# Optimization experiments

Hardware: AMD Instinct MI355X
Metric: run time of the kernel (lower is better)

## Reference

```python
import jax, jax.numpy as jnp
import numpy as np

B, N, HID, H = 16, 256, 512, 8
DK = HID // H          # att_size = 64
FEAT = 8               # storage/operator feature dim
MLP_H = 64             # interaction MLP hidden dim
LAM = 0.1              # htap_lambda
SCALE = DK ** -0.5


def _pair_bias(feat, W1, b1, W2, b2):
    """MLP([v_i || v_j || |v_i - v_j|]) for all pairs -> [B,N,N,H].
    Split W1 over the three concat blocks so the per-node parts are O(N)."""
    F = feat.shape[-1]
    Wa, Wb, Wc = W1[:F], W1[F:2 * F], W1[2 * F:]
    hi = feat @ Wa                                    # [B,N,MLP_H]
    hj = feat @ Wb                                    # [B,N,MLP_H]
    diff = jnp.abs(feat[:, :, None, :] - feat[:, None, :, :])  # [B,N,N,F]
    h = jax.nn.relu(hi[:, :, None, :] + hj[:, None, :, :] + diff @ Wc + b1)
    return h @ W2 + b2                                # [B,N,N,H]


def setup_inputs() -> dict:
    key = jax.random.key(0)
    ks = jax.random.split(key, 24)
    g = lambda i, shape, s=0.05: jax.random.normal(ks[i], shape, jnp.float32) * (1.0 if s is None else 1.0) * (s / 0.05 * 0.05 if False else 1.0)
    def w(i, shape, scale):
        return jax.random.normal(ks[i], shape, jnp.float32) * scale
    inp = {
        "q": w(0, (B, N, HID), 1.0),
        "k": w(1, (B, N, HID), 1.0),
        "v": w(2, (B, N, HID), 1.0),
        "tree_attn_bias": w(3, (B, H, N, N), 1.0),
        "storage_features": w(4, (B, N, FEAT), 1.0),
        "operator_features": w(5, (B, N, FEAT), 1.0),
        # attention projections (stored as [in,out])
        "Wq": w(6, (HID, HID), HID ** -0.5), "bq": jnp.zeros((HID,), jnp.float32),
        "Wk": w(7, (HID, HID), HID ** -0.5), "bk": jnp.zeros((HID,), jnp.float32),
        "Wv": w(8, (HID, HID), HID ** -0.5), "bv": jnp.zeros((HID,), jnp.float32),
        "Wo": w(9, (HID, HID), HID ** -0.5), "bo": jnp.zeros((HID,), jnp.float32),
        # f_s interaction MLP: Linear(3*FEAT,64) -> ReLU -> Linear(64,H)
        "fs_W1": w(10, (3 * FEAT, MLP_H), (3 * FEAT) ** -0.5), "fs_b1": jnp.zeros((MLP_H,), jnp.float32),
        "fs_W2": w(11, (MLP_H, H), MLP_H ** -0.5), "fs_b2": jnp.zeros((H,), jnp.float32),
        # f_o interaction MLP
        "fo_W1": w(12, (3 * FEAT, MLP_H), (3 * FEAT) ** -0.5), "fo_b1": jnp.zeros((MLP_H,), jnp.float32),
        "fo_W2": w(13, (MLP_H, H), MLP_H ** -0.5), "fo_b2": jnp.zeros((H,), jnp.float32),
    }
    return inp


def reference(q, k, v, tree_attn_bias, storage_features, operator_features,
              Wq, bq, Wk, bk, Wv, bv, Wo, bo,
              fs_W1, fs_b1, fs_W2, fs_b2, fo_W1, fo_b1, fo_W2, fo_b2):
    # projections -> [B,H,N,DK]
    qh = (q @ Wq + bq).reshape(B, N, H, DK).transpose(0, 2, 1, 3) * SCALE
    kh = (k @ Wk + bk).reshape(B, N, H, DK).transpose(0, 2, 1, 3)
    vh = (v @ Wv + bv).reshape(B, N, H, DK).transpose(0, 2, 1, 3)

    scores = jnp.einsum("bhnd,bhmd->bhnm", qh, kh) + tree_attn_bias

    htap = (_pair_bias(storage_features, fs_W1, fs_b1, fs_W2, fs_b2)
            + _pair_bias(operator_features, fo_W1, fo_b1, fo_W2, fo_b2))  # [B,N,N,H]
    scores = scores + LAM * htap.transpose(0, 3, 1, 2)

    attn = jax.nn.softmax(scores, axis=-1)            # dropout rate 0 (eval)
    x = jnp.einsum("bhnm,bhmd->bhnd", attn, vh)
    x = x.transpose(0, 2, 1, 3).reshape(B, N, HID)
    return x @ Wo + bo
```

## Files before the change

kernel.cpp:

```cpp
#include <hip/hip_runtime.h>
#include <hip/hip_bf16.h>
#include <stdint.h>

#define B_    16
#define N_    256
#define HID_  512
#define H_    8
#define DK_   64
#define FEAT_ 8
#define MLPH_ 64
#define LAM_  0.1f
#define SCALE_ 0.125f

typedef short bf16x8 __attribute__((ext_vector_type(8)));
typedef float f32x4  __attribute__((ext_vector_type(4)));

union U8 { uint4 u; bf16x8 h; ushort s[8]; };

__device__ __forceinline__ uint16_t f32_to_bf16(float x) {
    uint32_t u = __float_as_uint(x);
    u += 0x7fffu + ((u >> 16) & 1u);
    return (uint16_t)(u >> 16);
}
__device__ __forceinline__ float bf16_to_f32(uint16_t v) {
    return __uint_as_float(((uint32_t)v) << 16);
}
__device__ __forceinline__ uint32_t pk_bf16(float lo, float hi) {
    float2 xy; xy.x = lo; xy.y = hi;
    __hip_bfloat162 b2 = __float22bfloat162_rn(xy);
    return *(uint32_t*)&b2;
}
#define LDS_FENCE() asm volatile("s_waitcnt lgkmcnt(0)" ::: "memory")

__global__ __launch_bounds__(256, 4) void proj_kernel(
    const float* __restrict__ q, const float* __restrict__ k, const float* __restrict__ v,
    const float* __restrict__ Wq, const float* __restrict__ bq,
    const float* __restrict__ Wk, const float* __restrict__ bk,
    const float* __restrict__ Wv, const float* __restrict__ bv,
    ushort* __restrict__ qh, ushort* __restrict__ kh, ushort* __restrict__ vh)
{
    int z = blockIdx.z;
    const float* X    = (z == 0) ? q  : (z == 1) ? k  : v;
    const float* W    = (z == 0) ? Wq : (z == 1) ? Wk : Wv;
    const float* bias = (z == 0) ? bq : (z == 1) ? bk : bv;
    ushort* out       = (z == 0) ? qh : (z == 1) ? kh : vh;
    float scale       = (z == 0) ? SCALE_ : 1.0f;

    int m0 = blockIdx.x * 64;
    int h  = blockIdx.y;
    int c0 = h * 64;

    __shared__ __align__(16) ushort Xs[64 * 40];
    __shared__ __align__(16) ushort Ws[64 * 40];

    int t = threadIdx.x;
    int wave = t >> 6, lane = t & 63;
    int l15 = lane & 15, qd = lane >> 4;

    f32x4 acc[4] = {};

    for (int k0 = 0; k0 < HID_; k0 += 32) {
        __syncthreads();
        #pragma unroll
        for (int u = t; u < 512; u += 256) {
            int r = u >> 3, c4 = (u & 7) * 4;
            float4 xv = *(const float4*)&X[(m0 + r) * HID_ + k0 + c4];
            ushort4 o;
            o.x = f32_to_bf16(xv.x); o.y = f32_to_bf16(xv.y);
            o.z = f32_to_bf16(xv.z); o.w = f32_to_bf16(xv.w);
            *(ushort4*)&Xs[r * 40 + c4] = o;
        }
        {
            int kr = t & 15, nq = t >> 4;
            float4 w0 = *(const float4*)&W[(k0 + 2 * kr) * HID_ + c0 + nq * 4];
            float4 w1 = *(const float4*)&W[(k0 + 2 * kr + 1) * HID_ + c0 + nq * 4];
            const float* a0 = &w0.x; const float* a1 = &w1.x;
            #pragma unroll
            for (int i = 0; i < 4; i++) {
                uint32_t pk = (uint32_t)f32_to_bf16(a0[i]) | ((uint32_t)f32_to_bf16(a1[i]) << 16);
                *(uint32_t*)&Ws[(nq * 4 + i) * 40 + 2 * kr] = pk;
            }
        }
        __syncthreads();
        bf16x8 af = *(const bf16x8*)&Xs[(wave * 16 + l15) * 40 + qd * 8];
        #pragma unroll
        for (int nt = 0; nt < 4; nt++) {
            bf16x8 bf = *(const bf16x8*)&Ws[(nt * 16 + l15) * 40 + qd * 8];
            acc[nt] = __builtin_amdgcn_mfma_f32_16x16x32_bf16(af, bf, acc[nt], 0, 0, 0);
        }
    }

    #pragma unroll
    for (int nt = 0; nt < 4; nt++) {
        float bb = bias[c0 + nt * 16 + l15];
        #pragma unroll
        for (int r = 0; r < 4; r++) {
            int m = m0 + wave * 16 + qd * 4 + r;
            int b_ = m >> 8, n_ = m & 255;
            float val = (acc[nt][r] + bb) * scale;
            out[(((b_ * H_ + h) * N_) + n_) * DK_ + nt * 16 + l15] = f32_to_bf16(val);
        }
    }
}

__global__ void prep_frags(const float* __restrict__ fsW1, const float* __restrict__ foW1,
                           const float* __restrict__ fsW2, const float* __restrict__ foW2,
                           uint4* __restrict__ bfrag1, uint4* __restrict__ bfrag2)
{
    int t = threadIdx.x;
    #pragma unroll
    for (int e = t; e < 512; e += 256) {
        int nt = e >> 6, lane = e & 63, l15 = lane & 15, qd = lane >> 4;
        int n = nt * 16 + l15;
        ushort vals[8];
        #pragma unroll
        for (int u = 0; u < 8; u++) {
            float x = 0.f;
            if (n < 64) {
                if (qd == 0) x = fsW1[(16 + u) * 64 + n];
                else if (qd == 1) x = fsW1[(8 + u) * 64 + n];
            } else {
                int n2 = n - 64;
                if (qd == 2) x = foW1[(16 + u) * 64 + n2];
                else if (qd == 3) x = foW1[(8 + u) * 64 + n2];
            }
            vals[u] = f32_to_bf16(x);
        }
        uint4 pk;
        pk.x = (uint32_t)vals[0] | ((uint32_t)vals[1] << 16);
        pk.y = (uint32_t)vals[2] | ((uint32_t)vals[3] << 16);
        pk.z = (uint32_t)vals[4] | ((uint32_t)vals[5] << 16);
        pk.w = (uint32_t)vals[6] | ((uint32_t)vals[7] << 16);
        bfrag1[e] = pk;
    }
    {
        int e = t;
        int ks = e >> 6, lane = e & 63, l15 = lane & 15, qd = lane >> 4;
        ushort vals[8];
        #pragma unroll
        for (int u = 0; u < 8; u++) {
            float x = 0.f;
            if (l15 < 8) {
                int k2 = ks * 32 + qd * 8 + u;
                int c = ((k2 & 7) << 4) | (k2 >> 3);
                x = LAM_ * ((c < 64) ? fsW2[c * 8 + l15] : foW2[(c - 64) * 8 + l15]);
            }
            vals[u] = f32_to_bf16(x);
        }
        uint4 pk;
        pk.x = (uint32_t)vals[0] | ((uint32_t)vals[1] << 16);
        pk.y = (uint32_t)vals[2] | ((uint32_t)vals[3] << 16);
        pk.z = (uint32_t)vals[4] | ((uint32_t)vals[5] << 16);
        pk.w = (uint32_t)vals[6] | ((uint32_t)vals[7] << 16);
        bfrag2[e] = pk;
    }
}

#define HSTRIDE 136
__global__ __launch_bounds__(256, 4) void pair_bias_mfma(
    const float* __restrict__ sf, const float* __restrict__ of,
    const float* __restrict__ fsW1, const float* __restrict__ fsb1,
    const float* __restrict__ foW1, const float* __restrict__ fob1,
    const float* __restrict__ fsb2, const float* __restrict__ fob2,
    const uint4* __restrict__ bfrag1, const uint4* __restrict__ bfrag2,
    ushort* __restrict__ mlpb)
{
    __shared__ __align__(16) ushort hbuf[4][16 * HSTRIDE];
    __shared__ float hisbuf[128];
    __shared__ __align__(4) ushort tbuf[4][8 * 16];

    int i = blockIdx.x, b = blockIdx.y;
    int t = threadIdx.x;
    int wave = t >> 6, lane = t & 63;
    int l15 = lane & 15, qd = lane >> 4;

    if (t < 128) {
        int set = t >> 6, kk = t & 63;
        const float* W1 = set ? foW1 : fsW1;
        const float* fi = (set ? of : sf) + (b * N_ + i) * FEAT_;
        float a = (set ? fob1 : fsb1)[kk];
        #pragma unroll
        for (int f = 0; f < FEAT_; f++) a += fi[f] * W1[f * 64 + kk];
        hisbuf[t] = a;
    }

    bf16x8 Bf1[8], Bf2[4];
    #pragma unroll
    for (int nt = 0; nt < 8; nt++) { U8 u; u.u = bfrag1[nt * 64 + lane]; Bf1[nt] = u.h; }
    #pragma unroll
    for (int ks = 0; ks < 4; ks++) { U8 u; u.u = bfrag2[ks * 64 + lane]; Bf2[ks] = u.h; }

    const float* fsr = sf + (b * N_ + i) * FEAT_;
    const float* forr = of + (b * N_ + i) * FEAT_;
    float fsi[8], foi[8];
    #pragma unroll
    for (int u = 0; u < 8; u++) { fsi[u] = fsr[u]; foi[u] = forr[u]; }
    float b2l = LAM_ * (fsb2[l15 & 7] + fob2[l15 & 7]);

    __syncthreads();

    float hv[8];
    #pragma unroll
    for (int nt = 0; nt < 8; nt++) hv[nt] = hisbuf[nt * 16 + l15];

    ushort* hb = hbuf[wave];
    #pragma unroll
    for (int qt = 0; qt < 4; qt++) {
        int j0 = (wave * 4 + qt) * 16;
        int j = j0 + l15;

        const float* fr = ((qd < 2) ? sf : of) + (b * N_ + j) * FEAT_;
        float4 f0 = *(const float4*)&fr[0];
        float4 f1 = *(const float4*)&fr[4];
        float vals[8] = {f0.x, f0.y, f0.z, f0.w, f1.x, f1.y, f1.z, f1.w};
        if ((qd & 1) == 0) {
            const float* fi = (qd < 2) ? fsi : foi;
            #pragma unroll
            for (int u = 0; u < 8; u++) vals[u] = fabsf(vals[u] - fi[u]);
        }
        U8 au;
        #pragma unroll
        for (int p = 0; p < 4; p++)
            ((uint32_t*)&au)[p] = pk_bf16(vals[2 * p], vals[2 * p + 1]);
        bf16x8 af = au.h;

        f32x4 S1[8];
        #pragma unroll
        for (int nt = 0; nt < 8; nt++) {
            f32x4 c0 = {hv[nt], hv[nt], hv[nt], hv[nt]};
            S1[nt] = __builtin_amdgcn_mfma_f32_16x16x32_bf16(af, Bf1[nt], c0, 0, 0, 0);
        }

        #pragma unroll
        for (int r = 0; r < 4; r++) {
            uint4 w;
            w.x = pk_bf16(fmaxf(S1[0][r], 0.f), fmaxf(S1[1][r], 0.f));
            w.y = pk_bf16(fmaxf(S1[2][r], 0.f), fmaxf(S1[3][r], 0.f));
            w.z = pk_bf16(fmaxf(S1[4][r], 0.f), fmaxf(S1[5][r], 0.f));
            w.w = pk_bf16(fmaxf(S1[6][r], 0.f), fmaxf(S1[7][r], 0.f));
            *(uint4*)&hb[(qd * 4 + r) * HSTRIDE + l15 * 8] = w;
        }
        LDS_FENCE();

        f32x4 S2 = {b2l, b2l, b2l, b2l};
        #pragma unroll
        for (int ks = 0; ks < 4; ks++) {
            bf16x8 a2 = *(const bf16x8*)&hb[l15 * HSTRIDE + ks * 32 + qd * 8];
            S2 = __builtin_amdgcn_mfma_f32_16x16x32_bf16(a2, Bf2[ks], S2, 0, 0, 0);
        }

        if (l15 < 8) {
            #pragma unroll
            for (int r = 0; r < 4; r++)
                tbuf[wave][l15 * 16 + qd * 4 + r] = f32_to_bf16(S2[r]);
        }
        LDS_FENCE();

        {
            int h2 = lane >> 3, jp = lane & 7;
            uint32_t lo = tbuf[wave][h2 * 16 + jp * 2];
            uint32_t hi = tbuf[wave][h2 * 16 + jp * 2 + 1];
            uint32_t pk = lo | (hi << 16);
            *(uint32_t*)&mlpb[(((size_t)(b * H_ + h2) * N_ + i) * N_) + j0 + jp * 2] = pk;
        }
    }
}

__global__ __launch_bounds__(256, 2) void attn_kernel(
    const ushort* __restrict__ qh, const ushort* __restrict__ kh,
    const ushort* __restrict__ vh, const float* __restrict__ tree,
    const ushort* __restrict__ mlpb, ushort* __restrict__ ctxb)
{
    __shared__ __align__(16) ushort bufKP[256 * 72];
    __shared__ __align__(16) ushort bufV[64 * 264];

    int blk = blockIdx.x;
    int bh = blk >> 2;
    int quarter = blk & 3;

    int t = threadIdx.x;
    int wave = t >> 6, lane = t & 63;
    int l15 = lane & 15, qd = lane >> 4;
    int i0w = quarter * 64 + wave * 16;

    const ushort* khb = kh + (size_t)bh * N_ * DK_;
    const ushort* vhb = vh + (size_t)bh * N_ * DK_;

    #pragma unroll
    for (int u = t; u < 2048; u += 256) {
        int j = u >> 3, seg = (u & 7) * 8;
        uint4 kv = *(const uint4*)&khb[j * DK_ + seg];
        *(uint4*)&bufKP[j * 72 + seg] = kv;
    }
    #pragma unroll
    for (int u = t; u < 1024; u += 256) {
        int rp = u & 127, d0 = (u >> 7) * 8;
        U8 v0, v1;
        v0.u = *(const uint4*)&vhb[(2 * rp) * DK_ + d0];
        v1.u = *(const uint4*)&vhb[(2 * rp + 1) * DK_ + d0];
        #pragma unroll
        for (int jj = 0; jj < 8; jj++) {
            uint32_t pk = (uint32_t)v0.s[jj] | ((uint32_t)v1.s[jj] << 16);
            *(uint32_t*)&bufV[(d0 + jj) * 264 + 2 * rp] = pk;
        }
    }
    __syncthreads();

    bf16x8 a0, a1;
    {
        size_t qb = ((size_t)bh * N_ + i0w + l15) * DK_;
        U8 t0, t1;
        t0.u = *(const uint4*)&qh[qb + qd * 8];
        t1.u = *(const uint4*)&qh[qb + 32 + qd * 8];
        a0 = t0.h; a1 = t1.h;
    }
    f32x4 S[16];
    #pragma unroll
    for (int nt = 0; nt < 16; nt++) {
        f32x4 acc = {};
        bf16x8 b0 = *(const bf16x8*)&bufKP[(nt * 16 + l15) * 72 + qd * 8];
        bf16x8 b1 = *(const bf16x8*)&bufKP[(nt * 16 + l15) * 72 + 32 + qd * 8];
        acc = __builtin_amdgcn_mfma_f32_16x16x32_bf16(a0, b0, acc, 0, 0, 0);
        acc = __builtin_amdgcn_mfma_f32_16x16x32_bf16(a1, b1, acc, 0, 0, 0);
        S[nt] = acc;
    }

    {
        size_t base = ((size_t)bh * N_ + i0w + qd * 4) * N_ + l15;
        const float*  tr = tree + base;
        const ushort* mb = mlpb + base;
        #pragma unroll
        for (int nt = 0; nt < 16; nt++)
            #pragma unroll
            for (int r = 0; r < 4; r++)
                S[nt][r] += tr[(size_t)r * N_ + nt * 16] + bf16_to_f32(mb[(size_t)r * N_ + nt * 16]);
    }

    float mx[4], sm[4];
    #pragma unroll
    for (int r = 0; r < 4; r++) mx[r] = -1e30f;
    #pragma unroll
    for (int nt = 0; nt < 16; nt++)
        #pragma unroll
        for (int r = 0; r < 4; r++) mx[r] = fmaxf(mx[r], S[nt][r]);
    #pragma unroll
    for (int r = 0; r < 4; r++) {
        #pragma unroll
        for (int m = 1; m <= 8; m <<= 1) mx[r] = fmaxf(mx[r], __shfl_xor(mx[r], m));
    }
    #pragma unroll
    for (int r = 0; r < 4; r++) sm[r] = 0.f;
    #pragma unroll
    for (int nt = 0; nt < 16; nt++)
        #pragma unroll
        for (int r = 0; r < 4; r++) {
            float e = __expf(S[nt][r] - mx[r]);
            S[nt][r] = e;
            sm[r] += e;
        }
    #pragma unroll
    for (int r = 0; r < 4; r++) {
        #pragma unroll
        for (int m = 1; m <= 8; m <<= 1) sm[r] += __shfl_xor(sm[r], m);
        sm[r] = 1.0f / sm[r];
    }

    __syncthreads();

    {
        uint32_t* Pw = (uint32_t*)&bufKP[wave * 16 * 264];
        #pragma unroll
        for (int nt = 0; nt < 16; nt++)
            #pragma unroll
            for (int r = 0; r < 4; r++) {
                float p = S[nt][r] * sm[r];
                float po = __shfl_xor(p, 1);
                uint32_t pk = (uint32_t)f32_to_bf16(p) | ((uint32_t)f32_to_bf16(po) << 16);
                if ((lane & 1) == 0)
                    Pw[(qd * 4 + r) * 132 + nt * 8 + (l15 >> 1)] = pk;
            }
    }
    __syncthreads();

    const ushort* Pw = &bufKP[wave * 16 * 264];
    f32x4 O[4] = {};
    #pragma unroll
    for (int ks = 0; ks < 8; ks++) {
        int j0 = ks * 32;
        bf16x8 pa = *(const bf16x8*)&Pw[l15 * 264 + j0 + qd * 8];
        #pragma unroll
        for (int ntd = 0; ntd < 4; ntd++) {
            bf16x8 vb = *(const bf16x8*)&bufV[(ntd * 16 + l15) * 264 + j0 + qd * 8];
            O[ntd] = __builtin_amdgcn_mfma_f32_16x16x32_bf16(pa, vb, O[ntd], 0, 0, 0);
        }
    }

    #pragma unroll
    for (int ntd = 0; ntd < 4; ntd++)
        #pragma unroll
        for (int r = 0; r < 4; r++)
            ctxb[((size_t)bh * N_ + i0w + qd * 4 + r) * DK_ + ntd * 16 + l15] =
                f32_to_bf16(O[ntd][r]);
}

__global__ __launch_bounds__(256, 4) void outproj_kernel(
    const ushort* __restrict__ ctxb, const float* __restrict__ Wo,
    const float* __restrict__ bo, float* __restrict__ out)
{
    int m0 = blockIdx.x * 64;
    int c0 = blockIdx.y * 64;

    __shared__ __align__(16) ushort Xs[64 * 40];
    __shared__ __align__(16) ushort Ws[64 * 40];

    int t = threadIdx.x;
    int wave = t >> 6, lane = t & 63;
    int l15 = lane & 15, qd = lane >> 4;

    f32x4 acc[4] = {};

    for (int k0 = 0; k0 < HID_; k0 += 32) {
        __syncthreads();
        {
            int r = t >> 2, s8 = (t & 3) * 8;
            int m = m0 + r, b_ = m >> 8, n_ = m & 255;
            uint4 xv = *(const uint4*)&ctxb[(((b_ * H_ + (k0 >> 6)) * N_) + n_) * DK_ + (k0 & 63) + s8];
            *(uint4*)&Xs[r * 40 + s8] = xv;
        }
        {
            int kr = t & 15, nq = t >> 4;
            float4 w0 = *(const float4*)&Wo[(k0 + 2 * kr) * HID_ + c0 + nq * 4];
            float4 w1 = *(const float4*)&Wo[(k0 + 2 * kr + 1) * HID_ + c0 + nq * 4];
            const float* a0 = &w0.x; const float* a1 = &w1.x;
            #pragma unroll
            for (int i = 0; i < 4; i++) {
                uint32_t pk = (uint32_t)f32_to_bf16(a0[i]) | ((uint32_t)f32_to_bf16(a1[i]) << 16);
                *(uint32_t*)&Ws[(nq * 4 + i) * 40 + 2 * kr] = pk;
            }
        }
        __syncthreads();
        bf16x8 af = *(const bf16x8*)&Xs[(wave * 16 + l15) * 40 + qd * 8];
        #pragma unroll
        for (int nt = 0; nt < 4; nt++) {
            bf16x8 bf = *(const bf16x8*)&Ws[(nt * 16 + l15) * 40 + qd * 8];
            acc[nt] = __builtin_amdgcn_mfma_f32_16x16x32_bf16(af, bf, acc[nt], 0, 0, 0);
        }
    }

    #pragma unroll
    for (int nt = 0; nt < 4; nt++) {
        float bb = bo[c0 + nt * 16 + l15];
        #pragma unroll
        for (int r = 0; r < 4; r++) {
            int m = m0 + wave * 16 + qd * 4 + r;
            out[m * HID_ + c0 + nt * 16 + l15] = acc[nt][r] + bb;
        }
    }
}

extern "C" void kernel_launch(void* const* d_in, const int* in_sizes, int n_in,
                              void* d_out, int out_size, void* d_ws, size_t ws_size,
                              hipStream_t stream)
{
    const float* q    = (const float*)d_in[0];
    const float* k    = (const float*)d_in[1];
    const float* v    = (const float*)d_in[2];
    const float* tree = (const float*)d_in[3];
    const float* sf   = (const float*)d_in[4];
    const float* of   = (const float*)d_in[5];
    const float* Wq   = (const float*)d_in[6];
    const float* bq   = (const float*)d_in[7];
    const float* Wk   = (const float*)d_in[8];
    const float* bk   = (const float*)d_in[9];
    const float* Wv   = (const float*)d_in[10];
    const float* bv   = (const float*)d_in[11];
    const float* Wo   = (const float*)d_in[12];
    const float* bo   = (const float*)d_in[13];
    const float* fsW1 = (const float*)d_in[14];
    const float* fsb1 = (const float*)d_in[15];
    const float* fsW2 = (const float*)d_in[16];
    const float* fsb2 = (const float*)d_in[17];
    const float* foW1 = (const float*)d_in[18];
    const float* fob1 = (const float*)d_in[19];
    const float* foW2 = (const float*)d_in[20];
    const float* fob2 = (const float*)d_in[21];

    char* ws = (char*)d_ws;
    ushort* qh     = (ushort*)(ws + 0);
    ushort* kh     = (ushort*)(ws + 4194304);
    ushort* vh     = (ushort*)(ws + 8388608);
    ushort* ctxb   = (ushort*)(ws + 12582912);
    uint4*  bfrag1 = (uint4*)(ws + 16777216);
    uint4*  bfrag2 = (uint4*)(ws + 16785408);
    ushort* mlpb   = (ushort*)(ws + 23080960);

    proj_kernel<<<dim3(64, 8, 3), 256, 0, stream>>>(q, k, v, Wq, bq, Wk, bk, Wv, bv, qh, kh, vh);
    prep_frags<<<1, 256, 0, stream>>>(fsW1, foW1, fsW2, foW2, bfrag1, bfrag2);
    pair_bias_mfma<<<dim3(N_, B_), 256, 0, stream>>>(sf, of, fsW1, fsb1, foW1, fob1,
                                                     fsb2, fob2, bfrag1, bfrag2, mlpb);
    attn_kernel<<<512, 256, 0, stream>>>(qh, kh, vh, tree, mlpb, ctxb);
    outproj_kernel<<<dim3(64, 8), 256, 0, stream>>>(ctxb, Wo, bo, (float*)d_out);
}
```

Baseline: 233.9 us.

## Double-buffer projection GEMM with register prefetch and 128-row tiles

The QKV projection kernel now prefetches the next K-slice of X and W into registers while the current slice is consumed from a double-buffered LDS tile, which removes one barrier per iteration. The M tile grows from 64 to 128 rows, so each wave computes two 16-row MFMA fragments and reuses each W fragment twice. This halves the grid and raises register and LDS use per block, which may lower occupancy.

```diff
diff --git a/kernel.cpp b/kernel.cpp
--- a/kernel.cpp
+++ b/kernel.cpp
@@ -46,47 +46,64 @@
     ushort* out       = (z == 0) ? qh : (z == 1) ? kh : vh;
     float scale       = (z == 0) ? SCALE_ : 1.0f;
 
-    int m0 = blockIdx.x * 64;
+    int m0 = blockIdx.x * 128;
     int h  = blockIdx.y;
     int c0 = h * 64;
 
-    __shared__ __align__(16) ushort Xs[64 * 40];
-    __shared__ __align__(16) ushort Ws[64 * 40];
+    __shared__ __align__(16) ushort Xs[2][128 * 40];
+    __shared__ __align__(16) ushort Ws[2][64 * 40];
 
     int t = threadIdx.x;
     int wave = t >> 6, lane = t & 63;
     int l15 = lane & 15, qd = lane >> 4;
 
-    f32x4 acc[4] = {};
+    int xr = t >> 1, xc = (t & 1) * 16;
+    int kr = t & 15, nq = t >> 4;
+
+    f32x4 acc0[4] = {}, acc1[4] = {};
+
+    float4 xv[4], w0, w1;
+    #pragma unroll
+    for (int p = 0; p < 4; p++)
+        xv[p] = *(const float4*)&X[(m0 + xr) * HID_ + xc + p * 4];
+    w0 = *(const float4*)&W[(2 * kr) * HID_ + c0 + nq * 4];
+    w1 = *(const float4*)&W[(2 * kr + 1) * HID_ + c0 + nq * 4];
 
     for (int k0 = 0; k0 < HID_; k0 += 32) {
-        __syncthreads();
-        #pragma unroll
-        for (int u = t; u < 512; u += 256) {
-            int r = u >> 3, c4 = (u & 7) * 4;
-            float4 xv = *(const float4*)&X[(m0 + r) * HID_ + k0 + c4];
+        int buf = (k0 >> 5) & 1;
+        #pragma unroll
+        for (int p = 0; p < 4; p++) {
             ushort4 o;
-            o.x = f32_to_bf16(xv.x); o.y = f32_to_bf16(xv.y);
-            o.z = f32_to_bf16(xv.z); o.w = f32_to_bf16(xv.w);
-            *(ushort4*)&Xs[r * 40 + c4] = o;
+            o.x = f32_to_bf16(xv[p].x); o.y = f32_to_bf16(xv[p].y);
+            o.z = f32_to_bf16(xv[p].z); o.w = f32_to_bf16(xv[p].w);
+            *(ushort4*)&Xs[buf][xr * 40 + xc + p * 4] = o;
         }
         {
-            int kr = t & 15, nq = t >> 4;
-            float4 w0 = *(const float4*)&W[(k0 + 2 * kr) * HID_ + c0 + nq * 4];
-            float4 w1 = *(const float4*)&W[(k0 + 2 * kr + 1) * HID_ + c0 + nq * 4];
             const float* a0 = &w0.x; const float* a1 = &w1.x;
             #pragma unroll
             for (int i = 0; i < 4; i++) {
                 uint32_t pk = (uint32_t)f32_to_bf16(a0[i]) | ((uint32_t)f32_to_bf16(a1[i]) << 16);
-                *(uint32_t*)&Ws[(nq * 4 + i) * 40 + 2 * kr] = pk;
+                *(uint32_t*)&Ws[buf][(nq * 4 + i) * 40 + 2 * kr] = pk;
             }
         }
         __syncthreads();
-        bf16x8 af = *(const bf16x8*)&Xs[(wave * 16 + l15) * 40 + qd * 8];
+
+        if (k0 + 32 < HID_) {
+            int kn = k0 + 32;
+            #pragma unroll
+            for (int p = 0; p < 4; p++)
+                xv[p] = *(const float4*)&X[(m0 + xr) * HID_ + kn + xc + p * 4];
+            w0 = *(const float4*)&W[(kn + 2 * kr) * HID_ + c0 + nq * 4];
+            w1 = *(const float4*)&W[(kn + 2 * kr + 1) * HID_ + c0 + nq * 4];
+        }
+
+        bf16x8 af0 = *(const bf16x8*)&Xs[buf][(wave * 32 + l15) * 40 + qd * 8];
+        bf16x8 af1 = *(const bf16x8*)&Xs[buf][(wave * 32 + 16 + l15) * 40 + qd * 8];
         #pragma unroll
         for (int nt = 0; nt < 4; nt++) {
-            bf16x8 bf = *(const bf16x8*)&Ws[(nt * 16 + l15) * 40 + qd * 8];
-            acc[nt] = __builtin_amdgcn_mfma_f32_16x16x32_bf16(af, bf, acc[nt], 0, 0, 0);
+            bf16x8 bf = *(const bf16x8*)&Ws[buf][(nt * 16 + l15) * 40 + qd * 8];
+            acc0[nt] = __builtin_amdgcn_mfma_f32_16x16x32_bf16(af0, bf, acc0[nt], 0, 0, 0);
+            acc1[nt] = __builtin_amdgcn_mfma_f32_16x16x32_bf16(af1, bf, acc1[nt], 0, 0, 0);
         }
     }
 
@@ -94,11 +111,15 @@
     for (int nt = 0; nt < 4; nt++) {
         float bb = bias[c0 + nt * 16 + l15];
         #pragma unroll
-        for (int r = 0; r < 4; r++) {
-            int m = m0 + wave * 16 + qd * 4 + r;
-            int b_ = m >> 8, n_ = m & 255;
-            float val = (acc[nt][r] + bb) * scale;
-            out[(((b_ * H_ + h) * N_) + n_) * DK_ + nt * 16 + l15] = f32_to_bf16(val);
+        for (int g = 0; g < 2; g++) {
+            const f32x4& a = g ? acc1[nt] : acc0[nt];
+            #pragma unroll
+            for (int r = 0; r < 4; r++) {
+                int m = m0 + wave * 32 + g * 16 + qd * 4 + r;
+                int b_ = m >> 8, n_ = m & 255;
+                float val = (a[r] + bb) * scale;
+                out[(((b_ * H_ + h) * N_) + n_) * DK_ + nt * 16 + l15] = f32_to_bf16(val);
+            }
         }
     }
 }
@@ -494,7 +515,7 @@
     uint4*  bfrag2 = (uint4*)(ws + 16785408);
     ushort* mlpb   = (ushort*)(ws + 23080960);
 
-    proj_kernel<<<dim3(64, 8, 3), 256, 0, stream>>>(q, k, v, Wq, bq, Wk, bk, Wv, bv, qh, kh, vh);
+    proj_kernel<<<dim3(32, 8, 3), 256, 0, stream>>>(q, k, v, Wq, bq, Wk, bk, Wv, bv, qh, kh, vh);
     prep_frags<<<1, 256, 0, stream>>>(fsW1, foW1, fsW2, foW2, bfrag1, bfrag2);
     pair_bias_mfma<<<dim3(N_, B_), 256, 0, stream>>>(sf, of, fsW1, fsb1, foW1, fob1,
                                                      fsb2, fob2, bfrag1, bfrag2, mlpb);
```

Result: faster. 228.1 us (-2.5%).
